# Performance work log

Hardware: AMD Instinct MI355X
Metric: run time of the kernel (lower is better)

Reference implementation:

```python
import jax, jax.numpy as jnp
import numpy as np

N = 100000
E = 1600000
IN_DIM, HID, H_IN, OUT_DIM, H_OUT = 128, 32, 2, 1, 1
NEG_SLOPE = 0.2


def gat_conv(x, W, a_src, a_dst, b, src, dst, concat):
    """PyG-style GATConv. x:[N,F_in], W:[F_in,H*C], a_*:[H,C], b:[H*C] or [C]."""
    H, C = a_src.shape
    h = (x @ W).reshape(N, H, C)
    asrc = jnp.einsum('nhc,hc->nh', h, a_src)   # [N,H]
    adst = jnp.einsum('nhc,hc->nh', h, a_dst)   # [N,H]
    e = jax.nn.leaky_relu(asrc[src] + adst[dst], NEG_SLOPE)  # [E',H]
    # segment softmax over incoming edges of each destination node
    m = jax.ops.segment_max(e, dst, num_segments=N)
    p = jnp.exp(e - m[dst])
    s = jax.ops.segment_sum(p, dst, num_segments=N)
    alpha = p / s[dst]                           # [E',H]
    out = jax.ops.segment_sum(alpha[:, :, None] * h[src], dst, num_segments=N)  # [N,H,C]
    out = out.reshape(N, H * C) if concat else out.mean(axis=1)
    return out + b


def setup_inputs() -> dict:
    key = jax.random.key(0)
    ks = jax.random.split(key, 16)
    def glorot(k, shape):
        fan = sum(shape[-2:]) if len(shape) > 1 else shape[-1]
        return jax.random.normal(k, shape, jnp.float32) * (2.0 / fan) ** 0.5
    node_attrs = jax.random.normal(ks[0], (N, IN_DIM), jnp.float32)
    edge_index = jax.random.randint(ks[1], (2, E), 0, N, jnp.int64 if jax.config.jax_enable_x64 else jnp.int32)
    params = {
        'W_in':  glorot(ks[2], (IN_DIM, H_IN * HID)),
        'a_src_in': glorot(ks[3], (H_IN, HID)),
        'a_dst_in': glorot(ks[4], (H_IN, HID)),
        'b_in':  jnp.zeros((H_IN * HID,), jnp.float32),
        'W_mid': glorot(ks[5], (H_IN * HID, H_IN * HID)),
        'a_src_mid': glorot(ks[6], (H_IN, HID)),
        'a_dst_mid': glorot(ks[7], (H_IN, HID)),
        'b_mid': jnp.zeros((H_IN * HID,), jnp.float32),
        'W_out': glorot(ks[8], (H_IN * HID, H_OUT * OUT_DIM)),
        'a_src_out': glorot(ks[9], (H_OUT, OUT_DIM)),
        'a_dst_out': glorot(ks[10], (H_OUT, OUT_DIM)),
        'b_out': jnp.zeros((OUT_DIM,), jnp.float32),
    }
    return {'node_attrs': node_attrs, 'edge_index': edge_index, **params}


def reference(node_attrs, edge_index,
              W_in, a_src_in, a_dst_in, b_in,
              W_mid, a_src_mid, a_dst_mid, b_mid,
              W_out, a_src_out, a_dst_out, b_out):
    # add self loops (PyG GATConv default add_self_loops=True)
    loops = jnp.arange(N, dtype=edge_index.dtype)
    src = jnp.concatenate([edge_index[0], loops])
    dst = jnp.concatenate([edge_index[1], loops])

    x = gat_conv(node_attrs, W_in, a_src_in, a_dst_in, b_in, src, dst, True)
    initial_x = x
    x = jax.nn.elu(x)
    for _ in range(6):  # conv_mid reused 6 times with SHARED weights, as in source
        x = gat_conv(x, W_mid, a_src_mid, a_dst_mid, b_mid, src, dst, True) + initial_x
        x = jax.nn.elu(x)
    x = gat_conv(x, W_out, a_src_out, a_dst_out, b_out, src, dst, False)
    return jax.nn.sigmoid(x)
```

## Files before the change

kernel.cpp:

```cpp
#include <hip/hip_runtime.h>
#include <hip/hip_fp16.h>
#include <cmath>

#define NN 100000
#define EE 1600000
#define TOTE (EE + NN)
#define SHIFT 10
#define NBUK 98
#define CAPB 18432
#define SLACK 5632
#define SPAN (TOTE + NBUK * SLACK)
#define PCAP2 40


typedef _Float16 half8_t __attribute__((ext_vector_type(8)));
typedef _Float16 half4_t __attribute__((ext_vector_type(4)));
typedef float float4_t __attribute__((ext_vector_type(4)));

__device__ __forceinline__ float lrelu(float v) { return v > 0.f ? v : 0.2f * v; }

__global__ __launch_bounds__(256) void binA(const int* __restrict__ src, const int* __restrict__ dst,
                                            int* __restrict__ gcur, int* __restrict__ region) {
    __shared__ int cnt[NBUK], gbase[NBUK], pos[NBUK];
    int t = threadIdx.x;
    if (t < NBUK) cnt[t] = 0;
    __syncthreads();
    const int CH = (TOTE + gridDim.x - 1) / gridDim.x;
    int lo = blockIdx.x * CH;
    int hi = lo + CH; if (hi > TOTE) hi = TOTE;
    for (int e = lo + t; e < hi; e += 256) {
        int d = (e < EE) ? dst[e] : (e - EE);
        atomicAdd(&cnt[d >> SHIFT], 1);
    }
    __syncthreads();
    if (t < NBUK) {
        gbase[t] = atomicAdd(&gcur[t], cnt[t]);
        pos[t] = 0;
    }
    __syncthreads();
    for (int e = lo + t; e < hi; e += 256) {
        int s, d;
        if (e < EE) { s = src[e]; d = dst[e]; }
        else        { s = e - EE; d = s; }
        int b = d >> SHIFT;
        int k = atomicAdd(&pos[b], 1);
        region[(size_t)b * CAPB + gbase[b] + k] = (s << SHIFT) | (d & 1023);
    }
}

__global__ __launch_bounds__(1024) void binB(const int* __restrict__ region, const int* __restrict__ gcur,
                                             int2* __restrict__ rng, int* __restrict__ esrc) {
    __shared__ int ncur[1024];
    __shared__ int wsum[16];
    __shared__ int sg[NBUK];
    __shared__ int sBase;
    int b = blockIdx.x, t = threadIdx.x;
    int n0 = b << SHIFT;
    if (t < NBUK) sg[t] = gcur[t];
    ncur[t] = 0;
    __syncthreads();
    if (t == 0) {
        int run = 0;
        for (int bb = 0; bb < b; ++bb) run += sg[bb] + SLACK;
        sBase = run;
    }
    int cntE = gcur[b];
    const int* reg = region + (size_t)b * CAPB;
    __syncthreads();
    for (int i = t; i < cntE; i += 1024)
        atomicAdd(&ncur[reg[i] & 1023], 1);
    int base = sBase;
    __syncthreads();
    int v = ncur[t];
    int vp = (v + 7) & ~7;
    __syncthreads();
    int incl = vp;
    for (int off = 1; off < 64; off <<= 1) {
        int u = __shfl_up(incl, off);
        if ((t & 63) >= off) incl += u;
    }
    if ((t & 63) == 63) wsum[t >> 6] = incl;
    __syncthreads();
    if (t < 16) {
        int w = wsum[t];
        int winc = w;
        for (int off = 1; off < 16; off <<= 1) {
            int u = __shfl_up(winc, off);
            if (t >= off) winc += u;
        }
        wsum[t] = winc - w;
    }
    __syncthreads();
    int excl = incl - vp + wsum[t >> 6];
    int start = base + excl;
    int n = n0 + t;
    if (n < NN) rng[n] = make_int2(start, v);
    ncur[t] = start;
    __syncthreads();
    for (int i = t; i < cntE; i += 1024) {
        int p = reg[i];
        int local = p & 1023;
        int k = atomicAdd(&ncur[local], 1);
        esrc[k] = p >> SHIFT;
    }
    __syncthreads();
    if (n < NN) {
        for (int k = start + v; k < start + vp; ++k) esrc[k] = 0;
    }
}

__global__ __launch_bounds__(256) void degHist(const int2* __restrict__ rng, int* __restrict__ hist) {
    __shared__ int cnt[64];
    int t = threadIdx.x;
    if (t < 64) cnt[t] = 0;
    __syncthreads();
    int n = blockIdx.x * 256 + t;
    if (n < NN) {
        int d = rng[n].y; if (d > 63) d = 63;
        atomicAdd(&cnt[d], 1);
    }
    __syncthreads();
    if (t < 64 && cnt[t]) atomicAdd(&hist[t], cnt[t]);
}

__global__ void degScan(const int* __restrict__ hist, int* __restrict__ off) {
    int t = threadIdx.x;
    int v = hist[t];
    int incl = v;
    for (int o = 1; o < 64; o <<= 1) {
        int u = __shfl_up(incl, o);
        if (t >= o) incl += u;
    }
    off[t] = incl - v;
}

__global__ __launch_bounds__(256) void degSort(const int2* __restrict__ rng, int* __restrict__ off,
                                               int* __restrict__ perm) {
    __shared__ int cnt[64], base[64], pos[64];
    int t = threadIdx.x;
    if (t < 64) cnt[t] = 0;
    __syncthreads();
    int n = blockIdx.x * 256 + t;
    int d = 63;
    if (n < NN) {
        d = rng[n].y; if (d > 63) d = 63;
        atomicAdd(&cnt[d], 1);
    }
    __syncthreads();
    if (t < 64) { base[t] = atomicAdd(&off[t], cnt[t]); pos[t] = 0; }
    __syncthreads();
    if (n < NN) {
        int k = atomicAdd(&pos[d], 1);
        perm[base[d] + k] = n;
    }
}

template <int K, bool F32IN>
__global__ __launch_bounds__(256) void gemm_attn(const void* __restrict__ Xv, const float* __restrict__ W,
                                                 const float* __restrict__ a_src, const float* __restrict__ a_dst,
                                                 _Float16* __restrict__ H, float* __restrict__ asrc,
                                                 float* __restrict__ adst) {
    __shared__ _Float16 wt[64][K + 8];
    int t = threadIdx.x;
    for (int it = 0; it < K / 16; ++it) {
        int idx4 = it * 256 + t;
        int k = idx4 >> 4;
        int n4 = (idx4 * 4) & 63;
        int ks = F32IN ? k : ((k & 15) * 4 + (k >> 4));
        float4 v = *(const float4*)(W + (size_t)idx4 * 4);
        wt[n4 + 0][ks] = (_Float16)v.x;
        wt[n4 + 1][ks] = (_Float16)v.y;
        wt[n4 + 2][ks] = (_Float16)v.z;
        wt[n4 + 3][ks] = (_Float16)v.w;
    }
    __syncthreads();

    int row0 = blockIdx.x * 64;
    int wr = (t >> 6) * 16;
    int lane = t & 63;
    int m = lane & 15;
    int q = lane >> 4;

    int rowA = row0 + wr + m;
    if (rowA >= NN) rowA = NN - 1;

    float4_t acc[4] = { {0,0,0,0}, {0,0,0,0}, {0,0,0,0}, {0,0,0,0} };
#pragma unroll
    for (int kc = 0; kc < K / 32; ++kc) {
        half8_t av;
        if (F32IN) {
            const float* xrow = (const float*)Xv + (size_t)rowA * K + q * 8;
            float4 u0 = *(const float4*)(xrow + kc * 32);
            float4 u1 = *(const float4*)(xrow + kc * 32 + 4);
            av[0] = (_Float16)u0.x; av[1] = (_Float16)u0.y;
            av[2] = (_Float16)u0.z; av[3] = (_Float16)u0.w;
            av[4] = (_Float16)u1.x; av[5] = (_Float16)u1.y;
            av[6] = (_Float16)u1.z; av[7] = (_Float16)u1.w;
        } else {
            const _Float16* xrow = (const _Float16*)Xv + (size_t)rowA * K + q * 8;
            av = *(const half8_t*)(xrow + kc * 32);
        }
#pragma unroll
        for (int c = 0; c < 4; ++c) {
            half8_t bv = *(const half8_t*)&wt[c * 16 + m][kc * 32 + q * 8];
            acc[c] = __builtin_amdgcn_mfma_f32_16x16x32_f16(av, bv, acc[c], 0, 0, 0);
        }
    }

#pragma unroll
    for (int r = 0; r < 4; ++r) {
        int row = row0 + wr + q * 4 + r;
        if (row < NN) {
            half4_t hv = { (_Float16)acc[0][r], (_Float16)acc[1][r],
                           (_Float16)acc[2][r], (_Float16)acc[3][r] };
            *(half4_t*)(H + (size_t)row * 64 + m * 4) = hv;
        }
    }

    float as0 = a_src[m], as1 = a_src[16 + m], as2 = a_src[32 + m], as3 = a_src[48 + m];
    float ad0 = a_dst[m], ad1 = a_dst[16 + m], ad2 = a_dst[32 + m], ad3 = a_dst[48 + m];
#pragma unroll
    for (int r = 0; r < 4; ++r) {
        float s0 = acc[0][r] * as0 + acc[1][r] * as1;
        float s1 = acc[2][r] * as2 + acc[3][r] * as3;
        float d0 = acc[0][r] * ad0 + acc[1][r] * ad1;
        float d1 = acc[2][r] * ad2 + acc[3][r] * ad3;
#pragma unroll
        for (int mk = 1; mk < 16; mk <<= 1) {
            s0 += __shfl_xor(s0, mk);
            s1 += __shfl_xor(s1, mk);
            d0 += __shfl_xor(d0, mk);
            d1 += __shfl_xor(d1, mk);
        }
        int row = row0 + wr + q * 4 + r;
        if (m == 0 && row < NN) {
            asrc[2 * row + 0] = s0;
            asrc[2 * row + 1] = s1;
            adst[2 * row + 0] = d0;
            adst[2 * row + 1] = d1;
        }
    }
}

struct Acc8 { float a[8]; float l0, l1; };

__device__ __forceinline__ void acc4(Acc8& A, float4 p0, float4 p1, float4 p2, float4 p3,
                                     half8_t h0, half8_t h1, half8_t h2, half8_t h3) {
    A.l0 += p0.x + p1.x + p2.x + p3.x;
    A.l1 += p0.y + p1.y + p2.y + p3.y;
#pragma unroll
    for (int q = 0; q < 8; ++q) {
        float w0 = (q & 2) ? p0.y : p0.x;
        float w1 = (q & 2) ? p1.y : p1.x;
        float w2 = (q & 2) ? p2.y : p2.x;
        float w3 = (q & 2) ? p3.y : p3.x;
        A.a[q] += w0 * (float)h0[q] + w1 * (float)h1[q]
                + w2 * (float)h2[q] + w3 * (float)h3[q];
    }
}

template <int MODE>
__global__ __launch_bounds__(256) void edge_agg(const int* __restrict__ perm, const int2* __restrict__ rng,
                                                const int* __restrict__ esrc, const _Float16* __restrict__ h,
                                                const float* __restrict__ asrc, const float* __restrict__ adst,
                                                const float* __restrict__ bias, _Float16* __restrict__ ixbuf,
                                                _Float16* __restrict__ xout, const float* __restrict__ Wo,
                                                const float* __restrict__ a_s, const float* __restrict__ a_d,
                                                float2* __restrict__ ho2, float* __restrict__ adst_o) {
    __shared__ float4 pLDS[4][8][PCAP2 + 1];
    int bid = gridDim.x - 1 - blockIdx.x;
    int wq = threadIdx.x >> 6;
    int lane = threadIdx.x & 63;
    int g = lane >> 3;
    int c8 = lane & 7;
    int n = perm[(bid * 4 + wq) * 8 + g];
    int2 r = rng[n];
    int start = r.x, deg = r.y;
    int vp = (deg + 3) & ~3;
    if (vp > PCAP2) vp = PCAP2;
    float2 ad = *(const float2*)(adst + 2 * (size_t)n);

    for (int j = c8; j < vp; j += 8) {
        float p0 = 0.f, p1 = 0.f;
        int s = 0;
        if (j < deg) {
            s = esrc[start + j];
            float2 as = *(const float2*)(asrc + 2 * (size_t)s);
            p0 = __expf(fminf(lrelu(as.x + ad.x), 60.f));
            p1 = __expf(fminf(lrelu(as.y + ad.y), 60.f));
        }
        pLDS[wq][g][j] = make_float4(p0, p1, __int_as_float(s), 0.f);
    }

    float bi[8];
#pragma unroll
    for (int q = 0; q < 8; ++q) bi[q] = bias[(q & 3) * 16 + 2 * c8 + (q >> 2)];
    half8_t iv = {};
    if constexpr (MODE != 0) iv = *(const half8_t*)(ixbuf + (size_t)n * 64 + 8 * c8);
    float wo[8];
    float as0 = 0.f, ad0 = 0.f;
    if constexpr (MODE == 2) {
#pragma unroll
        for (int q = 0; q < 8; ++q) wo[q] = Wo[(q & 3) * 16 + 2 * c8 + (q >> 2)];
        as0 = a_s[0]; ad0 = a_d[0];
    }

    const float4* pb = &pLDS[wq][g][0];
    const _Float16* hb = h + 8 * c8;
    Acc8 A = {};
    float4 pc0 = pb[0], pc1 = pb[1], pc2 = pb[2], pc3 = pb[3];
    half8_t hc0 = *(const half8_t*)(hb + ((size_t)__float_as_int(pc0.z) << 6));
    half8_t hc1 = *(const half8_t*)(hb + ((size_t)__float_as_int(pc1.z) << 6));
    half8_t hc2 = *(const half8_t*)(hb + ((size_t)__float_as_int(pc2.z) << 6));
    half8_t hc3 = *(const half8_t*)(hb + ((size_t)__float_as_int(pc3.z) << 6));
    for (int j = 4; j < vp; j += 4) {
        float4 pn0 = pb[j], pn1 = pb[j + 1], pn2 = pb[j + 2], pn3 = pb[j + 3];
        acc4(A, pc0, pc1, pc2, pc3, hc0, hc1, hc2, hc3);
        half8_t hn0 = *(const half8_t*)(hb + ((size_t)__float_as_int(pn0.z) << 6));
        half8_t hn1 = *(const half8_t*)(hb + ((size_t)__float_as_int(pn1.z) << 6));
        half8_t hn2 = *(const half8_t*)(hb + ((size_t)__float_as_int(pn2.z) << 6));
        half8_t hn3 = *(const half8_t*)(hb + ((size_t)__float_as_int(pn3.z) << 6));
        pc0 = pn0; pc1 = pn1; pc2 = pn2; pc3 = pn3;
        hc0 = hn0; hc1 = hn1; hc2 = hn2; hc3 = hn3;
    }
    acc4(A, pc0, pc1, pc2, pc3, hc0, hc1, hc2, hc3);

    float inv0 = 1.f / A.l0, inv1 = 1.f / A.l1;
    float t[8];
#pragma unroll
    for (int q = 0; q < 8; ++q) t[q] = A.a[q] * ((q & 2) ? inv1 : inv0) + bi[q];
    if constexpr (MODE == 0) {
        half8_t o;
#pragma unroll
        for (int q = 0; q < 8; ++q) o[q] = (_Float16)t[q];
        *(half8_t*)(ixbuf + (size_t)n * 64 + 8 * c8) = o;
    } else {
#pragma unroll
        for (int q = 0; q < 8; ++q) t[q] += (float)iv[q];
    }
#pragma unroll
    for (int q = 0; q < 8; ++q) t[q] = t[q] > 0.f ? t[q] : __expf(t[q]) - 1.f;
    if constexpr (MODE != 2) {
        half8_t o;
#pragma unroll
        for (int q = 0; q < 8; ++q) o[q] = (_Float16)t[q];
        *(half8_t*)(xout + (size_t)n * 64 + 8 * c8) = o;
    } else {
        float v = 0.f;
#pragma unroll
        for (int q = 0; q < 8; ++q) v += t[q] * wo[q];
        v += __shfl_xor(v, 1);
        v += __shfl_xor(v, 2);
        v += __shfl_xor(v, 4);
        if (c8 == 0) {
            ho2[n] = make_float2(v, v * as0);
            adst_o[n] = v * ad0;
        }
    }
}

__global__ __launch_bounds__(256) void edge_agg_out(const int* __restrict__ perm, const int2* __restrict__ rng,
                                                    const int* __restrict__ esrc, const float2* __restrict__ ho2,
                                                    const float* __restrict__ adst_o, const float* __restrict__ b_out,
                                                    float* __restrict__ out) {
    int bid = gridDim.x - 1 - blockIdx.x;
    int wq = threadIdx.x >> 6;
    int lane = threadIdx.x & 63;
    int g = lane >> 3;
    int c8 = lane & 7;
    int n = perm[(bid * 4 + wq) * 8 + g];
    int2 r = rng[n];
    float adv = adst_o[n];
    float l = 0.f, acc = 0.f;
    for (int j = c8; j < r.y; j += 8) {
        int s = esrc[r.x + j];
        float2 v = ho2[s];
        float p = __expf(fminf(lrelu(v.y + adv), 60.f));
        l += p;
        acc = fmaf(p, v.x, acc);
    }
    l += __shfl_xor(l, 1); acc += __shfl_xor(acc, 1);
    l += __shfl_xor(l, 2); acc += __shfl_xor(acc, 2);
    l += __shfl_xor(l, 4); acc += __shfl_xor(acc, 4);
    if (c8 == 0) out[n] = 1.f / (1.f + __expf(-(acc / l + b_out[0])));
}

extern "C" void kernel_launch(void* const* d_in, const int* in_sizes, int n_in,
                              void* d_out, int out_size, void* d_ws, size_t ws_size,
                              hipStream_t stream) {
    const float* node_attrs = (const float*)d_in[0];
    const int*   edge_index = (const int*)d_in[1];
    const float* W_in      = (const float*)d_in[2];
    const float* a_src_in  = (const float*)d_in[3];
    const float* a_dst_in  = (const float*)d_in[4];
    const float* b_in      = (const float*)d_in[5];
    const float* W_mid     = (const float*)d_in[6];
    const float* a_src_mid = (const float*)d_in[7];
    const float* a_dst_mid = (const float*)d_in[8];
    const float* b_mid     = (const float*)d_in[9];
    const float* W_out     = (const float*)d_in[10];
    const float* a_src_out = (const float*)d_in[11];
    const float* a_dst_out = (const float*)d_in[12];
    const float* b_out     = (const float*)d_in[13];
    float* out = (float*)d_out;

    const int* srcArr = edge_index;
    const int* dstArr = edge_index + EE;

    char* w = (char*)d_ws;
    auto alloc = [&](size_t bytes) { void* p = (void*)w; w += (bytes + 255) & ~(size_t)255; return p; };
    int2*  rng        = (int2*)alloc((size_t)NN * 8);
    int*   gcur       = (int*)alloc((size_t)NBUK * 4);
    int*   region     = (int*)alloc((size_t)NBUK * CAPB * 4);
    int*   esrc       = (int*)alloc((size_t)SPAN * 4);
    _Float16* h       = (_Float16*)alloc((size_t)NN * 64 * 2);
    _Float16* x16     = (_Float16*)alloc((size_t)NN * 64 * 2);
    _Float16* ixbuf   = (_Float16*)alloc((size_t)NN * 64 * 2);
    float* asrc       = (float*)alloc((size_t)NN * 2 * 4);
    float* adst       = (float*)alloc((size_t)NN * 2 * 4);
    float2* ho2       = (float2*)alloc((size_t)NN * 8);
    float* adst_o     = (float*)alloc((size_t)NN * 4);
    int*   perm       = (int*)alloc((size_t)NN * 4);
    int*   hist       = (int*)alloc(64 * 4);
    int*   off        = (int*)alloc(64 * 4);

    hipMemsetAsync(gcur, 0, NBUK * 4, stream);
    hipMemsetAsync(hist, 0, 64 * 4, stream);
    binA<<<256, 256, 0, stream>>>(srcArr, dstArr, gcur, region);
    binB<<<NBUK, 1024, 0, stream>>>(region, gcur, rng, esrc);

    int nBlk = (NN + 255) / 256;
    degHist<<<nBlk, 256, 0, stream>>>(rng, hist);
    degScan<<<1, 64, 0, stream>>>(hist, off);
    degSort<<<nBlk, 256, 0, stream>>>(rng, off, perm);

    int gemmBlocks = (NN + 63) / 64;
    int aggBlocks = NN / 32;

    gemm_attn<128, true><<<gemmBlocks, 256, 0, stream>>>(node_attrs, W_in, a_src_in, a_dst_in, h, asrc, adst);
    edge_agg<0><<<aggBlocks, 256, 0, stream>>>(perm, rng, esrc, h, asrc, adst, b_in, ixbuf, x16,
                                               nullptr, nullptr, nullptr, nullptr, nullptr);

    for (int l = 0; l < 5; ++l) {
        gemm_attn<64, false><<<gemmBlocks, 256, 0, stream>>>(x16, W_mid, a_src_mid, a_dst_mid, h, asrc, adst);
        edge_agg<1><<<aggBlocks, 256, 0, stream>>>(perm, rng, esrc, h, asrc, adst, b_mid, ixbuf, x16,
                                                   nullptr, nullptr, nullptr, nullptr, nullptr);
    }
    gemm_attn<64, false><<<gemmBlocks, 256, 0, stream>>>(x16, W_mid, a_src_mid, a_dst_mid, h, asrc, adst);
    edge_agg<2><<<aggBlocks, 256, 0, stream>>>(perm, rng, esrc, h, asrc, adst, b_mid, ixbuf, nullptr,
                                               W_out, a_src_out, a_dst_out, ho2, adst_o);

    edge_agg_out<<<aggBlocks, 256, 0, stream>>>(perm, rng, esrc, ho2, adst_o, b_out, out);
}
```

Measured before the change: 563.3 us.

## Fuse next-layer GEMM and attention projections into edge aggregation epilogue

Each aggregation kernel now loads W_mid into LDS as fp16 and, after computing the ELU output for its 32 nodes, multiplies it by W_mid with MFMA instructions. It then writes the next layer's h, asrc and adst directly to ping-pong buffers. This removes six separate gemm_attn launches and the round trip of the x16 activation through global memory. In exchange, every block pays for a W staging pass, an extra __syncthreads, MFMA work and shuffle reductions, and it uses more LDS.

```diff
diff --git a/kernel.cpp b/kernel.cpp
--- a/kernel.cpp
+++ b/kernel.cpp
@@ -264,15 +264,35 @@
                                                 const int* __restrict__ esrc, const _Float16* __restrict__ h,
                                                 const float* __restrict__ asrc, const float* __restrict__ adst,
                                                 const float* __restrict__ bias, _Float16* __restrict__ ixbuf,
-                                                _Float16* __restrict__ xout, const float* __restrict__ Wo,
-                                                const float* __restrict__ a_s, const float* __restrict__ a_d,
-                                                float2* __restrict__ ho2, float* __restrict__ adst_o) {
+                                                const float* __restrict__ Wg, const float* __restrict__ asg,
+                                                const float* __restrict__ adg, _Float16* __restrict__ hN,
+                                                float* __restrict__ asrcN, float* __restrict__ adstN,
+                                                const float* __restrict__ Wo, const float* __restrict__ a_s,
+                                                const float* __restrict__ a_d, float2* __restrict__ ho2,
+                                                float* __restrict__ adst_o) {
     __shared__ float4 pLDS[4][8][PCAP2 + 1];
+    __shared__ _Float16 wt[(MODE != 2) ? 64 : 1][72];
     int bid = gridDim.x - 1 - blockIdx.x;
-    int wq = threadIdx.x >> 6;
-    int lane = threadIdx.x & 63;
+    int tid = threadIdx.x;
+    int wq = tid >> 6;
+    int lane = tid & 63;
     int g = lane >> 3;
     int c8 = lane & 7;
+
+    if constexpr (MODE != 2) {
+        for (int it = 0; it < 4; ++it) {
+            int idx4 = it * 256 + tid;
+            int k = idx4 >> 4;
+            int n4 = (idx4 * 4) & 63;
+            int ks = (k & 15) * 4 + (k >> 4);
+            float4 v = *(const float4*)(Wg + (size_t)idx4 * 4);
+            wt[n4 + 0][ks] = (_Float16)v.x;
+            wt[n4 + 1][ks] = (_Float16)v.y;
+            wt[n4 + 2][ks] = (_Float16)v.z;
+            wt[n4 + 3][ks] = (_Float16)v.w;
+        }
+    }
+
     int n = perm[(bid * 4 + wq) * 8 + g];
     int2 r = rng[n];
     int start = r.x, deg = r.y;
@@ -291,6 +311,7 @@
         }
         pLDS[wq][g][j] = make_float4(p0, p1, __int_as_float(s), 0.f);
     }
+    if constexpr (MODE != 2) __syncthreads();
 
     float bi[8];
 #pragma unroll
@@ -298,11 +319,11 @@
     half8_t iv = {};
     if constexpr (MODE != 0) iv = *(const half8_t*)(ixbuf + (size_t)n * 64 + 8 * c8);
     float wo[8];
-    float as0 = 0.f, ad0 = 0.f;
+    float as0o = 0.f, ad0o = 0.f;
     if constexpr (MODE == 2) {
 #pragma unroll
         for (int q = 0; q < 8; ++q) wo[q] = Wo[(q & 3) * 16 + 2 * c8 + (q >> 2)];
-        as0 = a_s[0]; ad0 = a_d[0];
+        as0o = a_s[0]; ad0o = a_d[0];
     }
 
     const float4* pb = &pLDS[wq][g][0];
@@ -340,11 +361,58 @@
     }
 #pragma unroll
     for (int q = 0; q < 8; ++q) t[q] = t[q] > 0.f ? t[q] : __expf(t[q]) - 1.f;
+
     if constexpr (MODE != 2) {
-        half8_t o;
-#pragma unroll
-        for (int q = 0; q < 8; ++q) o[q] = (_Float16)t[q];
-        *(half8_t*)(xout + (size_t)n * 64 + 8 * c8) = o;
+        _Float16* xs = (_Float16*)&pLDS[wq][0][0];
+        half8_t xv;
+#pragma unroll
+        for (int q = 0; q < 8; ++q) xv[q] = (_Float16)t[q];
+        *(half8_t*)(xs + g * 72 + 8 * c8) = xv;
+        int m = lane & 15, qq = lane >> 4;
+        const _Float16* xrow = xs + (m & 7) * 72 + qq * 8;
+        half8_t a0 = *(const half8_t*)(xrow);
+        half8_t a1 = *(const half8_t*)(xrow + 32);
+        float4_t ag[4] = { {0,0,0,0}, {0,0,0,0}, {0,0,0,0}, {0,0,0,0} };
+#pragma unroll
+        for (int c = 0; c < 4; ++c) {
+            half8_t b0 = *(const half8_t*)&wt[c * 16 + m][qq * 8];
+            half8_t b1 = *(const half8_t*)&wt[c * 16 + m][32 + qq * 8];
+            ag[c] = __builtin_amdgcn_mfma_f32_16x16x32_f16(a0, b0, ag[c], 0, 0, 0);
+            ag[c] = __builtin_amdgcn_mfma_f32_16x16x32_f16(a1, b1, ag[c], 0, 0, 0);
+        }
+        int base = (bid * 4 + wq) * 8;
+#pragma unroll
+        for (int rr = 0; rr < 4; ++rr) {
+            if (qq < 2) {
+                int nr = perm[base + qq * 4 + rr];
+                half4_t hv = { (_Float16)ag[0][rr], (_Float16)ag[1][rr],
+                               (_Float16)ag[2][rr], (_Float16)ag[3][rr] };
+                *(half4_t*)(hN + (size_t)nr * 64 + m * 4) = hv;
+            }
+        }
+        float gs0 = asg[m], gs1 = asg[16 + m], gs2 = asg[32 + m], gs3 = asg[48 + m];
+        float gd0 = adg[m], gd1 = adg[16 + m], gd2 = adg[32 + m], gd3 = adg[48 + m];
+#pragma unroll
+        for (int rr = 0; rr < 4; ++rr) {
+            float s0 = ag[0][rr] * gs0 + ag[1][rr] * gs1;
+            float s1 = ag[2][rr] * gs2 + ag[3][rr] * gs3;
+            float d0 = ag[0][rr] * gd0 + ag[1][rr] * gd1;
+            float d1 = ag[2][rr] * gd2 + ag[3][rr] * gd3;
+#pragma unroll
+            for (int mk = 1; mk < 16; mk <<= 1) {
+                s0 += __shfl_xor(s0, mk);
+                s1 += __shfl_xor(s1, mk);
+                d0 += __shfl_xor(d0, mk);
+                d1 += __shfl_xor(d1, mk);
+            }
+            if (m == 0 && qq < 2) {
+                int nr = perm[base + qq * 4 + rr];
+                asrcN[2 * nr + 0] = s0;
+                asrcN[2 * nr + 1] = s1;
+                adstN[2 * nr + 0] = d0;
+                adstN[2 * nr + 1] = d1;
+            }
+        }
     } else {
         float v = 0.f;
 #pragma unroll
@@ -353,8 +421,8 @@
         v += __shfl_xor(v, 2);
         v += __shfl_xor(v, 4);
         if (c8 == 0) {
-            ho2[n] = make_float2(v, v * as0);
-            adst_o[n] = v * ad0;
+            ho2[n] = make_float2(v, v * as0o);
+            adst_o[n] = v * ad0o;
         }
     }
 }
@@ -413,11 +481,13 @@
     int*   gcur       = (int*)alloc((size_t)NBUK * 4);
     int*   region     = (int*)alloc((size_t)NBUK * CAPB * 4);
     int*   esrc       = (int*)alloc((size_t)SPAN * 4);
-    _Float16* h       = (_Float16*)alloc((size_t)NN * 64 * 2);
-    _Float16* x16     = (_Float16*)alloc((size_t)NN * 64 * 2);
+    _Float16* hA      = (_Float16*)alloc((size_t)NN * 64 * 2);
+    _Float16* hB      = (_Float16*)alloc((size_t)NN * 64 * 2);
     _Float16* ixbuf   = (_Float16*)alloc((size_t)NN * 64 * 2);
-    float* asrc       = (float*)alloc((size_t)NN * 2 * 4);
-    float* adst       = (float*)alloc((size_t)NN * 2 * 4);
+    float* asA        = (float*)alloc((size_t)NN * 2 * 4);
+    float* adA        = (float*)alloc((size_t)NN * 2 * 4);
+    float* asB        = (float*)alloc((size_t)NN * 2 * 4);
+    float* adB        = (float*)alloc((size_t)NN * 2 * 4);
     float2* ho2       = (float2*)alloc((size_t)NN * 8);
     float* adst_o     = (float*)alloc((size_t)NN * 4);
     int*   perm       = (int*)alloc((size_t)NN * 4);
@@ -437,17 +507,21 @@
     int gemmBlocks = (NN + 63) / 64;
     int aggBlocks = NN / 32;
 
-    gemm_attn<128, true><<<gemmBlocks, 256, 0, stream>>>(node_attrs, W_in, a_src_in, a_dst_in, h, asrc, adst);
-    edge_agg<0><<<aggBlocks, 256, 0, stream>>>(perm, rng, esrc, h, asrc, adst, b_in, ixbuf, x16,
+    gemm_attn<128, true><<<gemmBlocks, 256, 0, stream>>>(node_attrs, W_in, a_src_in, a_dst_in, hA, asA, adA);
+
+    edge_agg<0><<<aggBlocks, 256, 0, stream>>>(perm, rng, esrc, hA, asA, adA, b_in, ixbuf,
+                                               W_mid, a_src_mid, a_dst_mid, hB, asB, adB,
                                                nullptr, nullptr, nullptr, nullptr, nullptr);
 
     for (int l = 0; l < 5; ++l) {
-        gemm_attn<64, false><<<gemmBlocks, 256, 0, stream>>>(x16, W_mid, a_src_mid, a_dst_mid, h, asrc, adst);
-        edge_agg<1><<<aggBlocks, 256, 0, stream>>>(perm, rng, esrc, h, asrc, adst, b_mid, ixbuf, x16,
+        _Float16* hs = (l & 1) ? hA : hB;  float* ass = (l & 1) ? asA : asB;  float* ads = (l & 1) ? adA : adB;
+        _Float16* hd = (l & 1) ? hB : hA;  float* asd = (l & 1) ? asB : asA;  float* add = (l & 1) ? adB : adA;
+        edge_agg<1><<<aggBlocks, 256, 0, stream>>>(perm, rng, esrc, hs, ass, ads, b_mid, ixbuf,
+                                                   W_mid, a_src_mid, a_dst_mid, hd, asd, add,
                                                    nullptr, nullptr, nullptr, nullptr, nullptr);
     }
-    gemm_attn<64, false><<<gemmBlocks, 256, 0, stream>>>(x16, W_mid, a_src_mid, a_dst_mid, h, asrc, adst);
-    edge_agg<2><<<aggBlocks, 256, 0, stream>>>(perm, rng, esrc, h, asrc, adst, b_mid, ixbuf, nullptr,
+    edge_agg<2><<<aggBlocks, 256, 0, stream>>>(perm, rng, esrc, hA, asA, adA, b_mid, ixbuf,
+                                               nullptr, nullptr, nullptr, nullptr, nullptr, nullptr,
                                                W_out, a_src_out, a_dst_out, ho2, adst_o);
 
     edge_agg_out<<<aggBlocks, 256, 0, stream>>>(perm, rng, esrc, ho2, adst_o, b_out, out);
```

Measured after the change: 521.0 us. -7.5%, faster.
